# Kernel optimization log

Hardware: AMD Instinct MI355X
Metric: run time of the kernel (lower is better)

Reference implementation:

```python
import jax, jax.numpy as jnp
import numpy as np
from jax import lax

B, C, H, W = 8, 256, 64, 64
A = 9                      # anchors per location (3 scales x 3 ratios)
STRIDE = 16
IMG = 1024                 # image_size
POST_NMS = 1000            # post_nms_top_n (also used as pre-NMS slice, as in source)
NMS_THR = 0.7
BBOX_XFORM_CLIP = 4.135166556742356  # log(1000/16)


def make_anchors():
    # ordering must match torch reshape (B,4,-1): index = a*H*W + h*W + w
    scales = jnp.array([128.0, 256.0, 512.0], dtype=jnp.float32)
    ratios = jnp.array([0.5, 1.0, 2.0], dtype=jnp.float32)
    ws = (scales[:, None] / jnp.sqrt(ratios)[None, :]).reshape(-1)  # [A]
    hs = (scales[:, None] * jnp.sqrt(ratios)[None, :]).reshape(-1)  # [A]
    cx = (jnp.arange(W, dtype=jnp.float32) + 0.5) * STRIDE
    cy = (jnp.arange(H, dtype=jnp.float32) + 0.5) * STRIDE
    cx = jnp.broadcast_to(cx[None, None, :], (A, H, W))
    cy = jnp.broadcast_to(cy[None, :, None], (A, H, W))
    aw = jnp.broadcast_to(ws[:, None, None], (A, H, W))
    ah = jnp.broadcast_to(hs[:, None, None], (A, H, W))
    anchors = jnp.stack([cx - aw / 2, cy - ah / 2, cx + aw / 2, cy + ah / 2], axis=-1)
    return anchors.reshape(-1, 4)  # [K,4] xyxy


def conv2d(x, w, b, pad):
    y = lax.conv_general_dilated(x, w, (1, 1), [(pad, pad), (pad, pad)],
                                 dimension_numbers=("NCHW", "OIHW", "NCHW"))
    return y + b[None, :, None, None]


def decode(t, anchors):
    # t: [K,4] (tx,ty,tw,th); anchors: [K,4] xyxy -> boxes xyxy
    aw = anchors[:, 2] - anchors[:, 0]
    ah = anchors[:, 3] - anchors[:, 1]
    acx = anchors[:, 0] + 0.5 * aw
    acy = anchors[:, 1] + 0.5 * ah
    cx = t[:, 0] * aw + acx
    cy = t[:, 1] * ah + acy
    w = jnp.exp(jnp.clip(t[:, 2], -BBOX_XFORM_CLIP, BBOX_XFORM_CLIP)) * aw
    h = jnp.exp(jnp.clip(t[:, 3], -BBOX_XFORM_CLIP, BBOX_XFORM_CLIP)) * ah
    return jnp.stack([cx - 0.5 * w, cy - 0.5 * h, cx + 0.5 * w, cy + 0.5 * h], axis=-1)


def box_iou(a, b):
    area_a = (a[:, 2] - a[:, 0]) * (a[:, 3] - a[:, 1])
    area_b = (b[:, 2] - b[:, 0]) * (b[:, 3] - b[:, 1])
    lt = jnp.maximum(a[:, None, :2], b[None, :, :2])
    rb = jnp.minimum(a[:, None, 2:], b[None, :, 2:])
    wh = jnp.clip(rb - lt, 0.0)
    inter = wh[..., 0] * wh[..., 1]
    return inter / (area_a[:, None] + area_b[None, :] - inter)


def filter_one(boxes, scores):
    # boxes [K,4], scores [K]. Faithful to source: torch.sort ascending,
    # slice to POST_NMS, then class-agnostic greedy NMS, pad to POST_NMS.
    order = jnp.argsort(lax.stop_gradient(scores))        # ascending (torch.sort default)
    idx = order[:POST_NMS]
    b = boxes[idx]
    s = scores[idx]
    # batched_nms internally processes boxes in descending-score order
    o2 = jnp.argsort(-lax.stop_gradient(s))
    b2 = b[o2]
    s2 = s[o2]
    iou = box_iou(b2, b2)  # [POST_NMS, POST_NMS]
    N = POST_NMS
    pos = jnp.arange(N)

    def body(i, keep):
        sup = (iou[i] > NMS_THR) & (pos > i) & keep[i]
        return keep & ~sup

    keep = lax.fori_loop(0, N, body, jnp.ones((N,), dtype=bool))
    # pack kept boxes (descending-score order) to the front, zero-pad the rest
    perm = jnp.argsort(jnp.where(keep, pos, N + pos))
    valid = pos < jnp.sum(keep)
    out_b = jnp.where(valid[:, None], b2[perm], 0.0)
    out_s = jnp.where(valid, s2[perm], 0.0)
    return out_b, out_s


def setup_inputs() -> dict:
    key = jax.random.key(0)
    ks = jax.random.split(key, 5)
    x = jax.random.normal(ks[0], (B, C, H, W), dtype=jnp.float32)
    conv_w = jax.random.normal(ks[1], (C, C, 3, 3), dtype=jnp.float32) * 0.01
    conv_b = jnp.zeros((C,), dtype=jnp.float32)
    box_w = jax.random.normal(ks[2], (4 * A, C, 1, 1), dtype=jnp.float32) * 0.01
    box_b = jnp.zeros((4 * A,), dtype=jnp.float32)
    obj_w = jax.random.normal(ks[3], (A, C, 1, 1), dtype=jnp.float32) * 0.01
    obj_b = jnp.zeros((A,), dtype=jnp.float32)
    return {"x": x, "conv_w": conv_w, "conv_b": conv_b,
            "box_w": box_w, "box_b": box_b, "obj_w": obj_w, "obj_b": obj_b}


def reference(x, conv_w, conv_b, box_w, box_b, obj_w, obj_b):
    feats = jax.nn.relu(conv2d(x, conv_w, conv_b, 1))        # [B,C,H,W]
    t = conv2d(feats, box_w, box_b, 0)                        # [B,4A,H,W]
    o = conv2d(feats, obj_w, obj_b, 0)                        # [B,A,H,W]
    t = t.reshape(B, 4, -1).transpose(0, 2, 1)                # [B,K,4]
    obj = o.reshape(B, -1)                                    # [B,K]
    anchors = make_anchors()                                  # [K,4]
    props = jax.vmap(lambda ti: decode(ti, anchors))(t)       # [B,K,4]
    props = jnp.clip(props, 0.0, float(IMG))                  # clip_boxes_to_image
    out_b, out_s = jax.vmap(filter_one)(props, obj)           # [B,POST_NMS,4],[B,POST_NMS]
    return jnp.concatenate([out_b, out_s[..., None]], axis=-1)  # [B,POST_NMS,5]
```

## Files before the change

### kernel.cpp

```cpp
#include <hip/hip_runtime.h>

#define B_ 8
#define C_ 256
#define H_ 64
#define W_ 64
#define HW_ 4096
#define HP_ 66
#define HWP_ 4224
#define A_ 9
#define SITES 36864
#define NPOST 1000
#define XCLIPF 4.1351666f
#define IMGF 1024.0f

__device__ inline unsigned keyf(float v) {
  unsigned u = __float_as_uint(v);
  return (u & 0x80000000u) ? ~u : (u | 0x80000000u);
}

__device__ __forceinline__ float dpp_shr1(float v) {
  return __int_as_float(__builtin_amdgcn_update_dpp(
      0, __float_as_int(v), 0x111 , 0xf, 0xf, true));
}
__device__ __forceinline__ float dpp_shl1(float v) {
  return __int_as_float(__builtin_amdgcn_update_dpp(
      0, __float_as_int(v), 0x101 , 0xf, 0xf, true));
}

__global__ __launch_bounds__(256) void pad_x(
    const float* __restrict__ x, float* __restrict__ xp) {
  int t = blockIdx.x * 256 + threadIdx.x;
  int c4 = t & 15;
  int rr = (t >> 4) % HP_;
  int bc = t / (HP_ * 16);
  float4 v = make_float4(0.f, 0.f, 0.f, 0.f);
  if (rr >= 1 && rr <= 64)
    v = ((const float4*)x)[(size_t)bc * (HW_ / 4) + (size_t)(rr - 1) * 16 + c4];
  ((float4*)xp)[(size_t)bc * (HWP_ / 4) + (size_t)rr * 16 + c4] = v;
}

__global__ __launch_bounds__(256) void pack_w(
    const float* __restrict__ w, float* __restrict__ wq) {
  int idx = blockIdx.x * 256 + threadIdx.x;
  int quad = idx / (256 * 36);
  int rem  = idx % (256 * 36);
  int ci = rem / 36;
  int k  = rem % 36;
  int q = k / 9, t = k % 9;
  wq[idx] = w[((size_t)(quad * 4 + q)) * (C_ * 9) + (size_t)ci * 9 + t];
}

__global__ __launch_bounds__(256, 2) void conv3_4co(
    const float* __restrict__ xp, const float* __restrict__ wq,
    const float* __restrict__ bias, float* __restrict__ feats) {
#pragma clang fp contract(off)
  int b       = blockIdx.x & 7;
  int j       = blockIdx.x >> 3;
  int quad    = j & 63;
  int quarter = j >> 6;
  int co0 = quad << 2;
  int row16 = threadIdx.x >> 4;
  int chunk = threadIdx.x & 15;
  int gr = (quarter << 4) + row16;
  int c0 = chunk << 2;

  const float* px0 = xp + (size_t)b * C_ * HWP_ + (size_t)gr * W_ + c0;
  const float* wqb = wq + (size_t)quad * (C_ * 36);

  float acc[4][4][9];
#pragma unroll
  for (int q = 0; q < 4; ++q)
#pragma unroll
    for (int p = 0; p < 4; ++p)
#pragma unroll
      for (int t = 0; t < 9; ++t) acc[q][p][t] = 0.f;

#pragma unroll 2
  for (int ci = 0; ci < C_; ++ci) {
    const float* pr = px0 + (size_t)ci * HWP_;
    float4 tA = ((const float4*)(pr      ))[0];
    float4 mA = ((const float4*)(pr +  64))[0];
    float4 bA = ((const float4*)(pr + 128))[0];

    float T[6], M[6], Bo[6];
    T[1]=tA.x;  T[2]=tA.y;  T[3]=tA.z;  T[4]=tA.w;
    M[1]=mA.x;  M[2]=mA.y;  M[3]=mA.z;  M[4]=mA.w;
    Bo[1]=bA.x; Bo[2]=bA.y; Bo[3]=bA.z; Bo[4]=bA.w;

    T[0]  = dpp_shr1(T[4]);   T[5]  = dpp_shl1(T[1]);
    M[0]  = dpp_shr1(M[4]);   M[5]  = dpp_shl1(M[1]);
    Bo[0] = dpp_shr1(Bo[4]);  Bo[5] = dpp_shl1(Bo[1]);

    const float* wrow = wqb + ci * 36;
    float w9[4][9];
#pragma unroll
    for (int q = 0; q < 4; ++q)
#pragma unroll
      for (int t = 0; t < 9; ++t) w9[q][t] = wrow[q * 9 + t];

#pragma unroll
    for (int q = 0; q < 4; ++q)
#pragma unroll
      for (int p = 0; p < 4; ++p) {
        acc[q][p][0] = fmaf(w9[q][0], T[p],     acc[q][p][0]);
        acc[q][p][1] = fmaf(w9[q][1], T[p+1],   acc[q][p][1]);
        acc[q][p][2] = fmaf(w9[q][2], T[p+2],   acc[q][p][2]);
        acc[q][p][3] = fmaf(w9[q][3], M[p],     acc[q][p][3]);
        acc[q][p][4] = fmaf(w9[q][4], M[p+1],   acc[q][p][4]);
        acc[q][p][5] = fmaf(w9[q][5], M[p+2],   acc[q][p][5]);
        acc[q][p][6] = fmaf(w9[q][6], Bo[p],    acc[q][p][6]);
        acc[q][p][7] = fmaf(w9[q][7], Bo[p+1],  acc[q][p][7]);
        acc[q][p][8] = fmaf(w9[q][8], Bo[p+2],  acc[q][p][8]);
      }
  }

#pragma unroll
  for (int q = 0; q < 4; ++q) {
    float bv = bias[co0 + q];
    float ov[4];
#pragma unroll
    for (int p = 0; p < 4; ++p) {
      float a = 0.f;
#pragma unroll
      for (int t = 0; t < 9; ++t) a = a + acc[q][p][t];
      a = a + bv;
      ov[p] = a > 0.f ? a : 0.f;
    }
    float4* fo = (float4*)(feats + ((size_t)b * C_ + co0 + q) * HW_ + (size_t)gr * W_ + c0);
    fo[0] = make_float4(ov[0], ov[1], ov[2], ov[3]);
  }
}

__global__ __launch_bounds__(256) void conv1_split3(
    const float* __restrict__ feats,
    const float* __restrict__ box_w, const float* __restrict__ box_b,
    const float* __restrict__ obj_w, const float* __restrict__ obj_b,
    float* __restrict__ tbox, float* __restrict__ scores) {
#pragma clang fp contract(off)
  int gidx = blockIdx.x * 256 + threadIdx.x;
  int cgrp = gidx >> 15;
  int rem  = gidx & 32767;
  int b  = rem >> 12;
  int hw = rem & 4095;
  int cbase = cgrp * 15;
  const float* f = feats + (size_t)b * C_ * HW_ + hw;
  const float* wrow[15];
#pragma unroll
  for (int jj = 0; jj < 15; ++jj) {
    int c = cbase + jj;
    wrow[jj] = (c < 36) ? (box_w + (size_t)c * C_) : (obj_w + (size_t)(c - 36) * C_);
  }
  float acc[15];
#pragma unroll
  for (int jj = 0; jj < 15; ++jj) acc[jj] = 0.f;
  for (int ci = 0; ci < C_; ++ci) {
    float fv = f[(size_t)ci * HW_];
#pragma unroll
    for (int jj = 0; jj < 15; ++jj)
      acc[jj] = fmaf(wrow[jj][ci], fv, acc[jj]);
  }
#pragma unroll
  for (int jj = 0; jj < 15; ++jj) {
    int c = cbase + jj;
    if (c < 36) {
      int k = c / 9, a = c - k * 9;
      tbox[(size_t)b * 4 * SITES + (size_t)k * SITES + (size_t)a * HW_ + hw] = acc[jj] + box_b[c];
    } else {
      int a = c - 36;
      scores[(size_t)b * SITES + (size_t)a * HW_ + hw] = acc[jj] + obj_b[a];
    }
  }
}

__global__ __launch_bounds__(1024) void select_sort_decode(
    const float* __restrict__ scores, const float* __restrict__ tbox,
    float* __restrict__ s2, float* __restrict__ b2) {
#pragma clang fp contract(off)
  int b = blockIdx.x;
  const float* s = scores + (size_t)b * SITES;
  __shared__ unsigned hist[256];
  __shared__ unsigned sh_prefix, sh_mask, sh_cless;
  __shared__ int sh_target;
  __shared__ int sh_cnt, sh_eq;
  __shared__ int sh_sel[1024];
  __shared__ int sh_eqList[4096];
  __shared__ float ss[NPOST];
  __shared__ int st[NPOST];
  if (threadIdx.x == 0) {
    sh_prefix = 0; sh_mask = 0; sh_target = NPOST - 1; sh_cless = 0;
    sh_cnt = 0; sh_eq = 0;
  }
  for (int shift = 24; shift >= 0; shift -= 8) {
    if (threadIdx.x < 256) hist[threadIdx.x] = 0;
    __syncthreads();
    unsigned prefix = sh_prefix, mask = sh_mask;
    for (int i = threadIdx.x; i < SITES; i += 1024) {
      unsigned k = keyf(s[i]);
      if ((k & mask) == prefix) atomicAdd(&hist[(k >> shift) & 255u], 1u);
    }
    __syncthreads();
    if (threadIdx.x == 0) {
      unsigned cum = 0; int t = sh_target; int v = 0;
      for (; v < 256; ++v) {
        unsigned h = hist[v];
        if (cum + h > (unsigned)t) break;
        cum += h;
      }
      sh_prefix |= ((unsigned)v) << shift;
      sh_mask   |= 0xFFu << shift;
      sh_target  = t - (int)cum;
      sh_cless  += cum;
    }
    __syncthreads();
  }
  unsigned K = sh_prefix;
  int need = NPOST - (int)sh_cless;
  for (int i = threadIdx.x; i < SITES; i += 1024) {
    unsigned k = keyf(s[i]);
    if (k < K) {
      int pos = atomicAdd(&sh_cnt, 1);
      sh_sel[pos] = i;
    } else if (k == K) {
      int e = atomicAdd(&sh_eq, 1);
      if (e < 4096) sh_eqList[e] = i;
    }
  }
  __syncthreads();
  {
    int E = sh_eq; if (E > 4096) E = 4096;
    int base = sh_cnt;
    for (int t = threadIdx.x; t < E; t += 1024) {
      int site = sh_eqList[t];
      int rank = 0;
      for (int q = 0; q < E; ++q) rank += (sh_eqList[q] < site);
      if (rank < need) sh_sel[base + rank] = site;
    }
  }
  __syncthreads();
  for (int t = threadIdx.x; t < NPOST; t += 1024) {
    int site = sh_sel[t];
    st[t] = site;
    ss[t] = s[site];
  }
  __syncthreads();
  if (threadIdx.x < NPOST) {
    int r = threadIdx.x;
    float sr = ss[r]; int sir = st[r];
    int d = 0;
    for (int q = 0; q < NPOST; ++q) {
      float sq = ss[q];
      d += (int)((sq > sr) || (sq == sr && st[q] < sir));
    }
    s2[(size_t)b * NPOST + d] = sr;
    int site = sir;
    int a = site / HW_;
    int hw = site - a * HW_;
    int h = hw / W_, wc = hw - h * W_;
    int sidx = a / 3, ridx = a - sidx * 3;
    float scale = (sidx == 0) ? 128.f : ((sidx == 1) ? 256.f : 512.f);
    float ratio = (ridx == 0) ? 0.5f : ((ridx == 1) ? 1.0f : 2.0f);
    float sq = sqrtf(ratio);
    float wsa = scale / sq;
    float hsa = scale * sq;
    float cx = ((float)wc + 0.5f) * 16.f;
    float cy = ((float)h + 0.5f) * 16.f;
    float ax1 = cx - wsa * 0.5f;
    float ay1 = cy - hsa * 0.5f;
    float ax2 = cx + wsa * 0.5f;
    float ay2 = cy + hsa * 0.5f;
    float aw = ax2 - ax1, ah = ay2 - ay1;
    float m1 = 0.5f * aw, m2 = 0.5f * ah;
    float acx = ax1 + m1, acy = ay1 + m2;
    const float* tb = tbox + (size_t)b * 4 * SITES + site;
    float t0 = tb[0];
    float t1 = tb[SITES];
    float t2 = tb[2 * (size_t)SITES];
    float t3 = tb[3 * (size_t)SITES];
    if (t2 < -XCLIPF) t2 = -XCLIPF;
    if (t2 > XCLIPF) t2 = XCLIPF;
    if (t3 < -XCLIPF) t3 = -XCLIPF;
    if (t3 > XCLIPF) t3 = XCLIPF;
    float pm0 = t0 * aw;  float pcx = pm0 + acx;
    float pm1 = t1 * ah;  float pcy = pm1 + acy;
    float pw = expf(t2) * aw;
    float ph = expf(t3) * ah;
    float hw0 = 0.5f * pw, hh0 = 0.5f * ph;
    float x1 = pcx - hw0, y1 = pcy - hh0;
    float x2 = pcx + hw0, y2 = pcy + hh0;
    x1 = x1 < 0.f ? 0.f : (x1 > IMGF ? IMGF : x1);
    y1 = y1 < 0.f ? 0.f : (y1 > IMGF ? IMGF : y1);
    x2 = x2 < 0.f ? 0.f : (x2 > IMGF ? IMGF : x2);
    y2 = y2 < 0.f ? 0.f : (y2 > IMGF ? IMGF : y2);
    float* o = b2 + ((size_t)b * NPOST + d) * 4;
    o[0] = x1; o[1] = y1; o[2] = x2; o[3] = y2;
  }
}

__global__ __launch_bounds__(256) void mask_kernel(
    const float* __restrict__ b2, unsigned long long* __restrict__ sup) {
#pragma clang fp contract(off)
  int b = blockIdx.x / 63;
  int i0 = (blockIdx.x % 63) * 16;
  __shared__ float bs[NPOST * 4];
  __shared__ float area[NPOST];
  for (int t = threadIdx.x; t < NPOST * 4; t += 256) bs[t] = b2[(size_t)b * NPOST * 4 + t];
  __syncthreads();
  for (int t = threadIdx.x; t < NPOST; t += 256)
    area[t] = (bs[t * 4 + 2] - bs[t * 4]) * (bs[t * 4 + 3] - bs[t * 4 + 1]);
  __syncthreads();
  int i = i0 + (threadIdx.x & 15);
  int wd = threadIdx.x >> 4;
  if (i >= NPOST) return;
  float ax1 = bs[i * 4], ay1 = bs[i * 4 + 1], ax2 = bs[i * 4 + 2], ay2 = bs[i * 4 + 3];
  float aa = area[i];
  unsigned long long m = 0;
  for (int bit = 0; bit < 64; ++bit) {
    int j = wd * 64 + bit;
    if (j > i && j < NPOST) {
      float lx = fmaxf(ax1, bs[j * 4]);
      float ly = fmaxf(ay1, bs[j * 4 + 1]);
      float rx = fminf(ax2, bs[j * 4 + 2]);
      float ry = fminf(ay2, bs[j * 4 + 3]);
      float iw = rx - lx; if (iw < 0.f) iw = 0.f;
      float ih = ry - ly; if (ih < 0.f) ih = 0.f;
      float inter = iw * ih;
      float denom = (aa + area[j]) - inter;
      float iou = inter / denom;
      if (iou > 0.7f) m |= 1ull << bit;
    }
  }
  sup[((size_t)b * NPOST + i) * 16 + wd] = m;
}

__global__ __launch_bounds__(64) void nms_out(
    const unsigned long long* __restrict__ sup, const float* __restrict__ b2,
    const float* __restrict__ s2, float* __restrict__ out) {
  int b = blockIdx.x;
  int lane = threadIdx.x;
  unsigned long long kw = 0;
  if (lane < 16) kw = (lane < 15) ? ~0ull : ((1ull << 40) - 1);
  const unsigned long long* ms = sup + (size_t)b * NPOST * 16;
  unsigned long long mb[8];
#pragma unroll
  for (int k = 0; k < 8; ++k)
    mb[k] = (lane < 16) ? ms[(size_t)k * 16 + lane] : 0ull;
  for (int i0 = 0; i0 < NPOST; i0 += 8) {
    unsigned long long nb[8];
#pragma unroll
    for (int k = 0; k < 8; ++k) {
      int nx = i0 + 8 + k;
      nb[k] = (nx < NPOST && lane < 16) ? ms[(size_t)nx * 16 + lane] : 0ull;
    }
#pragma unroll
    for (int k = 0; k < 8; ++k) {
      int i = i0 + k;
      unsigned long long w = __shfl(kw, i >> 6, 64);
      if ((w >> (i & 63)) & 1ull) {
        if (lane < 16) kw &= ~mb[k];
      }
    }
#pragma unroll
    for (int k = 0; k < 8; ++k) mb[k] = nb[k];
  }
  __shared__ unsigned long long keeps[16];
  if (lane < 16) keeps[lane] = kw;
  __syncthreads();
  int total = 0;
#pragma unroll
  for (int k = 0; k < 16; ++k) total += __popcll(keeps[k]);
  for (int i = lane; i < NPOST; i += 64) {
    int w = i >> 6;
    int before = 0;
    for (int k = 0; k < w; ++k) before += __popcll(keeps[k]);
    before += __popcll(keeps[w] & ((1ull << (i & 63)) - 1));
    bool kept = (keeps[w] >> (i & 63)) & 1ull;
    if (kept) {
      size_t ob = (size_t)b * (NPOST * 5) + (size_t)before * 5;
      const float* src = b2 + ((size_t)b * NPOST + i) * 4;
      out[ob + 0] = src[0];
      out[ob + 1] = src[1];
      out[ob + 2] = src[2];
      out[ob + 3] = src[3];
      out[ob + 4] = s2[(size_t)b * NPOST + i];
    }
    if (i >= total) {
      size_t ob = (size_t)b * (NPOST * 5) + (size_t)i * 5;
      for (int c = 0; c < 5; ++c) out[ob + c] = 0.f;
    }
  }
}

extern "C" void kernel_launch(void* const* d_in, const int* in_sizes, int n_in,
                              void* d_out, int out_size, void* d_ws, size_t ws_size,
                              hipStream_t stream) {
  const float *x = nullptr, *conv_w = nullptr, *conv_b = nullptr,
              *box_w = nullptr, *box_b = nullptr, *obj_w = nullptr, *obj_b = nullptr;
  for (int i = 0; i < n_in; ++i) {
    switch (in_sizes[i]) {
      case 8388608: x = (const float*)d_in[i]; break;
      case 589824:  conv_w = (const float*)d_in[i]; break;
      case 256:     conv_b = (const float*)d_in[i]; break;
      case 9216:    box_w = (const float*)d_in[i]; break;
      case 36:      box_b = (const float*)d_in[i]; break;
      case 2304:    obj_w = (const float*)d_in[i]; break;
      case 9:       obj_b = (const float*)d_in[i]; break;
    }
  }
  float* out = (float*)d_out;

  char* p = (char*)d_ws;
  auto alloc = [&](size_t n) { char* q = p; p += (n + 255) & ~255ull; return (void*)q; };
  float* feats  = (float*)alloc((size_t)B_ * C_ * HW_ * 4);
  float* tbox   = (float*)alloc((size_t)B_ * 4 * SITES * 4);
  float* scores = (float*)alloc((size_t)B_ * SITES * 4);
  float* xpad   = (float*)alloc((size_t)B_ * C_ * HWP_ * 4);
  float* wq     = (float*)alloc((size_t)64 * C_ * 36 * 4);
  float* s2     = (float*)alloc((size_t)B_ * NPOST * 4);
  float* b2     = (float*)alloc((size_t)B_ * NPOST * 4 * 4);
  unsigned long long* sup = (unsigned long long*)alloc((size_t)B_ * NPOST * 16 * 8);

  hipLaunchKernelGGL(pad_x, dim3(B_ * C_ * HP_ * 16 / 256), dim3(256), 0, stream, x, xpad);
  hipLaunchKernelGGL(pack_w, dim3(64 * C_ * 36 / 256), dim3(256), 0, stream, conv_w, wq);
  hipLaunchKernelGGL(conv3_4co, dim3(B_ * 64 * 4), dim3(256), 0, stream,
                     xpad, wq, conv_b, feats);
  hipLaunchKernelGGL(conv1_split3, dim3(3 * B_ * HW_ / 256), dim3(256), 0, stream,
                     feats, box_w, box_b, obj_w, obj_b, tbox, scores);
  hipLaunchKernelGGL(select_sort_decode, dim3(B_), dim3(1024), 0, stream,
                     scores, tbox, s2, b2);
  hipLaunchKernelGGL(mask_kernel, dim3(B_ * 63), dim3(256), 0, stream, b2, sup);
  hipLaunchKernelGGL(nms_out, dim3(B_), dim3(64), 0, stream, sup, b2, s2, out);
}
```

Before: 978.9 us.

## Merge prep kernels, compute all 45 head channels per thread, unroll conv loop

Merges the padding and weight-packing kernels into one prep launch, which also transposes the 1x1 head weights into a ci-major layout. The 1x1 head kernel now computes all 45 output channels per pixel, so each feature value is read once instead of three times, and it uses 64-thread blocks. The 3x3 conv inner loop unroll goes from 2 to 4. The 45 accumulators raise register pressure, the smaller head grid may lower occupancy, and the larger unroll may cause register spills.

```diff
diff --git a/kernel.cpp b/kernel.cpp
--- a/kernel.cpp
+++ b/kernel.cpp
@@ -27,27 +27,36 @@
       0, __float_as_int(v), 0x101 , 0xf, 0xf, true));
 }
 
-__global__ __launch_bounds__(256) void pad_x(
-    const float* __restrict__ x, float* __restrict__ xp) {
-  int t = blockIdx.x * 256 + threadIdx.x;
-  int c4 = t & 15;
-  int rr = (t >> 4) % HP_;
-  int bc = t / (HP_ * 16);
-  float4 v = make_float4(0.f, 0.f, 0.f, 0.f);
-  if (rr >= 1 && rr <= 64)
-    v = ((const float4*)x)[(size_t)bc * (HW_ / 4) + (size_t)(rr - 1) * 16 + c4];
-  ((float4*)xp)[(size_t)bc * (HWP_ / 4) + (size_t)rr * 16 + c4] = v;
-}
-
-__global__ __launch_bounds__(256) void pack_w(
-    const float* __restrict__ w, float* __restrict__ wq) {
-  int idx = blockIdx.x * 256 + threadIdx.x;
-  int quad = idx / (256 * 36);
-  int rem  = idx % (256 * 36);
-  int ci = rem / 36;
-  int k  = rem % 36;
-  int q = k / 9, t = k % 9;
-  wq[idx] = w[((size_t)(quad * 4 + q)) * (C_ * 9) + (size_t)ci * 9 + t];
+__global__ __launch_bounds__(256) void prep(
+    const float* __restrict__ x, const float* __restrict__ w,
+    const float* __restrict__ box_w, const float* __restrict__ obj_w,
+    float* __restrict__ xp, float* __restrict__ wq, float* __restrict__ wt) {
+  int blk = blockIdx.x;
+  if (blk < 8448) {
+    int t = blk * 256 + threadIdx.x;
+    int c4 = t & 15;
+    int rr = (t >> 4) % HP_;
+    int bc = t / (HP_ * 16);
+    float4 v = make_float4(0.f, 0.f, 0.f, 0.f);
+    if (rr >= 1 && rr <= 64)
+      v = ((const float4*)x)[(size_t)bc * (HW_ / 4) + (size_t)(rr - 1) * 16 + c4];
+    ((float4*)xp)[(size_t)bc * (HWP_ / 4) + (size_t)rr * 16 + c4] = v;
+  } else if (blk < 8448 + 2304) {
+    int idx = (blk - 8448) * 256 + threadIdx.x;
+    int quad = idx / (256 * 36);
+    int rem  = idx % (256 * 36);
+    int ci = rem / 36;
+    int k  = rem % 36;
+    int q = k / 9, t = k % 9;
+    wq[idx] = w[((size_t)(quad * 4 + q)) * (C_ * 9) + (size_t)ci * 9 + t];
+  } else {
+    int idx = (blk - 8448 - 2304) * 256 + threadIdx.x;
+    if (idx < C_ * 45) {
+      int ci = idx / 45, jj = idx % 45;
+      wt[idx] = (jj < 36) ? box_w[(size_t)jj * C_ + ci]
+                          : obj_w[(size_t)(jj - 36) * C_ + ci];
+    }
+  }
 }
 
 __global__ __launch_bounds__(256, 2) void conv3_4co(
@@ -75,7 +84,7 @@
 #pragma unroll
       for (int t = 0; t < 9; ++t) acc[q][p][t] = 0.f;
 
-#pragma unroll 2
+#pragma unroll 4
   for (int ci = 0; ci < C_; ++ci) {
     const float* pr = px0 + (size_t)ci * HWP_;
     float4 tA = ((const float4*)(pr      ))[0];
@@ -131,45 +140,34 @@
   }
 }
 
-__global__ __launch_bounds__(256) void conv1_split3(
-    const float* __restrict__ feats,
-    const float* __restrict__ box_w, const float* __restrict__ box_b,
-    const float* __restrict__ obj_w, const float* __restrict__ obj_b,
+__global__ __launch_bounds__(64) void conv1_all45(
+    const float* __restrict__ feats, const float* __restrict__ wt,
+    const float* __restrict__ box_b, const float* __restrict__ obj_b,
     float* __restrict__ tbox, float* __restrict__ scores) {
 #pragma clang fp contract(off)
-  int gidx = blockIdx.x * 256 + threadIdx.x;
-  int cgrp = gidx >> 15;
-  int rem  = gidx & 32767;
-  int b  = rem >> 12;
-  int hw = rem & 4095;
-  int cbase = cgrp * 15;
+  int gidx = blockIdx.x * 64 + threadIdx.x;
+  int b  = gidx >> 12;
+  int hw = gidx & 4095;
   const float* f = feats + (size_t)b * C_ * HW_ + hw;
-  const float* wrow[15];
-#pragma unroll
-  for (int jj = 0; jj < 15; ++jj) {
-    int c = cbase + jj;
-    wrow[jj] = (c < 36) ? (box_w + (size_t)c * C_) : (obj_w + (size_t)(c - 36) * C_);
-  }
-  float acc[15];
-#pragma unroll
-  for (int jj = 0; jj < 15; ++jj) acc[jj] = 0.f;
+  float acc[45];
+#pragma unroll
+  for (int jj = 0; jj < 45; ++jj) acc[jj] = 0.f;
+#pragma unroll 4
   for (int ci = 0; ci < C_; ++ci) {
     float fv = f[(size_t)ci * HW_];
-#pragma unroll
-    for (int jj = 0; jj < 15; ++jj)
-      acc[jj] = fmaf(wrow[jj][ci], fv, acc[jj]);
-  }
-#pragma unroll
-  for (int jj = 0; jj < 15; ++jj) {
-    int c = cbase + jj;
-    if (c < 36) {
-      int k = c / 9, a = c - k * 9;
-      tbox[(size_t)b * 4 * SITES + (size_t)k * SITES + (size_t)a * HW_ + hw] = acc[jj] + box_b[c];
-    } else {
-      int a = c - 36;
-      scores[(size_t)b * SITES + (size_t)a * HW_ + hw] = acc[jj] + obj_b[a];
-    }
-  }
+    const float* wr = wt + ci * 45;
+#pragma unroll
+    for (int jj = 0; jj < 45; ++jj)
+      acc[jj] = fmaf(wr[jj], fv, acc[jj]);
+  }
+#pragma unroll
+  for (int c = 0; c < 36; ++c) {
+    int k = c / 9, a = c - k * 9;
+    tbox[(size_t)b * 4 * SITES + (size_t)k * SITES + (size_t)a * HW_ + hw] = acc[c] + box_b[c];
+  }
+#pragma unroll
+  for (int a = 0; a < 9; ++a)
+    scores[(size_t)b * SITES + (size_t)a * HW_ + hw] = acc[36 + a] + obj_b[a];
 }
 
 __global__ __launch_bounds__(1024) void select_sort_decode(
@@ -415,16 +413,17 @@
   float* scores = (float*)alloc((size_t)B_ * SITES * 4);
   float* xpad   = (float*)alloc((size_t)B_ * C_ * HWP_ * 4);
   float* wq     = (float*)alloc((size_t)64 * C_ * 36 * 4);
+  float* wt     = (float*)alloc((size_t)C_ * 45 * 4);
   float* s2     = (float*)alloc((size_t)B_ * NPOST * 4);
   float* b2     = (float*)alloc((size_t)B_ * NPOST * 4 * 4);
   unsigned long long* sup = (unsigned long long*)alloc((size_t)B_ * NPOST * 16 * 8);
 
-  hipLaunchKernelGGL(pad_x, dim3(B_ * C_ * HP_ * 16 / 256), dim3(256), 0, stream, x, xpad);
-  hipLaunchKernelGGL(pack_w, dim3(64 * C_ * 36 / 256), dim3(256), 0, stream, conv_w, wq);
+  hipLaunchKernelGGL(prep, dim3(8448 + 2304 + 45), dim3(256), 0, stream,
+                     x, conv_w, box_w, obj_w, xpad, wq, wt);
   hipLaunchKernelGGL(conv3_4co, dim3(B_ * 64 * 4), dim3(256), 0, stream,
                      xpad, wq, conv_b, feats);
-  hipLaunchKernelGGL(conv1_split3, dim3(3 * B_ * HW_ / 256), dim3(256), 0, stream,
-                     feats, box_w, box_b, obj_w, obj_b, tbox, scores);
+  hipLaunchKernelGGL(conv1_all45, dim3(B_ * HW_ / 64), dim3(64), 0, stream,
+                     feats, wt, box_b, obj_b, tbox, scores);
   hipLaunchKernelGGL(select_sort_decode, dim3(B_), dim3(1024), 0, stream,
                      scores, tbox, s2, b2);
   hipLaunchKernelGGL(mask_kernel, dim3(B_ * 63), dim3(256), 0, stream, b2, sup);
```

Result: no change. 966.0 us (-1.3%).
